# Optimization experiments

Hardware: AMD Instinct MI355X
Metric: run time of the kernel (lower is better)

## Reference

```python
import jax, jax.numpy as jnp
import numpy as np

N = 100000
E = 1600000
IN_C, HID_C, OUT_C = 128, 128, 64


def setup_inputs() -> dict:
    key = jax.random.key(0)
    k1, k2, k3, k4 = jax.random.split(key, 4)
    x = jax.random.normal(k1, (N, IN_C), dtype=jnp.float32)
    edge_index = jax.random.randint(k2, (2, E), 0, N, dtype=jnp.int32)
    # Glorot-ish scaled weights
    W1 = jax.random.normal(k3, (IN_C, HID_C), dtype=jnp.float32) / np.sqrt(IN_C)
    b1 = jnp.zeros((HID_C,), dtype=jnp.float32)
    W2 = jax.random.normal(k4, (HID_C, OUT_C), dtype=jnp.float32) / np.sqrt(HID_C)
    b2 = jnp.zeros((OUT_C,), dtype=jnp.float32)
    return {"x": x, "edge_index": edge_index, "W1": W1, "b1": b1, "W2": W2, "b2": b2}


def _gcn_norm(edge_index, num_nodes):
    """Add self loops and compute symmetric D^{-1/2} A D^{-1/2} edge weights (PyG GCNConv defaults)."""
    loop = jnp.arange(num_nodes, dtype=edge_index.dtype)
    row = jnp.concatenate([edge_index[0], loop])  # source nodes
    col = jnp.concatenate([edge_index[1], loop])  # target nodes
    ones = jnp.ones_like(col, dtype=jnp.float32)
    deg = jax.ops.segment_sum(ones, col, num_segments=num_nodes)
    deg_inv_sqrt = jnp.where(deg > 0, jax.lax.rsqrt(jnp.maximum(deg, 1.0)), 0.0)
    norm = deg_inv_sqrt[row] * deg_inv_sqrt[col]  # [E+N]
    return row, col, norm


def _gcn_layer(x, row, col, norm, W, b, num_nodes):
    h = x @ W                                   # [N, C_out] transform first (PyG order)
    msg = h[row] * norm[:, None]                # gather + scale  [E+N, C_out]
    out = jax.ops.segment_sum(msg, col, num_segments=num_nodes)  # scatter-add
    return out + b


def reference(x, edge_index, W1, b1, W2, b2):
    row, col, norm = _gcn_norm(edge_index, N)
    h = jax.nn.relu(_gcn_layer(x, row, col, norm, W1, b1, N))
    return _gcn_layer(h, row, col, norm, W2, b2, N)
```

## Files before the change

kernel.cpp:

```cpp
#include <hip/hip_runtime.h>
#include <hip/hip_fp16.h>

#define NODES 100000
#define EDGES 1600000

#define BSHIFT 9
#define BNODES 512
#define NBUCK ((NODES + BNODES - 1) / BNODES)
#define BCAP 10240

#define GB 782
#define SC 1563

typedef __attribute__((ext_vector_type(8))) short short8;
typedef __attribute__((ext_vector_type(8))) _Float16 half8;
typedef __attribute__((ext_vector_type(4))) float f32x4;

__device__ inline unsigned short f2bf(float f) {
    unsigned u = __builtin_bit_cast(unsigned, f);
    u = u + 0x7fff + ((u >> 16) & 1);
    return (unsigned short)(u >> 16);
}
__device__ inline float bf2f(unsigned short h) {
    unsigned u = ((unsigned)h) << 16;
    return __builtin_bit_cast(float, u);
}
__device__ inline unsigned short f2h_bits(float f) {
    __half h = __float2half_rn(f);
    return __builtin_bit_cast(unsigned short, h);
}
__device__ inline float h2f(unsigned short bits) {
    return __half2float(__builtin_bit_cast(__half, bits));
}
__device__ inline float2 h2f2(unsigned int bits) {
    __half2 h = __builtin_bit_cast(__half2, bits);
    return __half22float2(h);
}


__global__ __launch_bounds__(256) void prep_kernel(const float* __restrict__ W1,
                                                   const float* __restrict__ W2,
                                                   unsigned short* __restrict__ wh1,
                                                   unsigned short* __restrict__ wl1,
                                                   unsigned short* __restrict__ w2f,
                                                   int* __restrict__ gcur) {
    const int tid = threadIdx.x;
    const int b = blockIdx.x;
    if (b < 8) {
        constexpr int NCT = 8;
        int idx = b * 256 + tid;
        int lane = idx & 63;
        int rem = idx >> 6;
        int ct = rem % NCT;
        int kt = rem / NCT;
        int kbase = kt * 32 + ((lane >> 4) * 8);
        int c = ct * 16 + (lane & 15);
#pragma unroll
        for (int i = 0; i < 8; i++) {
            float v = W1[(size_t)(kbase + i) * 128 + c];
            unsigned short hi = f2bf(v);
            unsigned short lo = f2bf(v - bf2f(hi));
            wh1[(size_t)idx * 8 + i] = hi;
            wl1[(size_t)idx * 8 + i] = lo;
        }
    } else if (b < 12) {
        constexpr int NCT = 4;
        int idx = (b - 8) * 256 + tid;
        int lane = idx & 63;
        int rem = idx >> 6;
        int ct = rem % NCT;
        int kt = rem / NCT;
        int kbase = kt * 32 + ((lane >> 4) * 8);
        int c = ct * 16 + (lane & 15);
#pragma unroll
        for (int i = 0; i < 8; i++) {
            w2f[(size_t)idx * 8 + i] = f2h_bits(W2[(size_t)(kbase + i) * 64 + c]);
        }
    } else {
        if (tid < NBUCK) gcur[tid] = 0;
    }
}


__device__ __forceinline__ void gemm1_body(const float* __restrict__ X,
                                           const unsigned short* __restrict__ wh,
                                           const unsigned short* __restrict__ wl,
                                           unsigned short* __restrict__ H,
                                           unsigned short* s_wh,
                                           unsigned short* s_wl,
                                           int tid, int bid) {
    constexpr int NCT = 8;
    constexpr int FRAGS = 2048;

    const int wave = tid >> 6;
    const int lane = tid & 63;

    const int row0 = bid * 128 + wave * 16 + (lane & 15);
    const bool active = (bid * 128 + wave * 16) < NODES;

    float xs[4][8];
    if (active) {
        const float* xrow = X + (size_t)row0 * 128 + ((lane >> 4) * 8);
#pragma unroll
        for (int kt = 0; kt < 4; kt++) {
            float4 a = *(const float4*)(xrow + kt * 32);
            float4 b = *(const float4*)(xrow + kt * 32 + 4);
            xs[kt][0] = a.x; xs[kt][1] = a.y; xs[kt][2] = a.z; xs[kt][3] = a.w;
            xs[kt][4] = b.x; xs[kt][5] = b.y; xs[kt][6] = b.z; xs[kt][7] = b.w;
        }
    }

#pragma unroll
    for (int j = 0; j < 4; j++) {
        __builtin_amdgcn_global_load_lds((const unsigned int*)((const char*)wh + ((size_t)tid + j * 512) * 16),
                                         (unsigned int*)(s_wh + ((size_t)tid + j * 512) * 8), 16, 0, 0);
        __builtin_amdgcn_global_load_lds((const unsigned int*)((const char*)wl + ((size_t)tid + j * 512) * 16),
                                         (unsigned int*)(s_wl + ((size_t)tid + j * 512) * 8), 16, 0, 0);
    }
    __syncthreads();

    if (!active) return;

    short8 ah[4], al[4];
#pragma unroll
    for (int kt = 0; kt < 4; kt++) {
#pragma unroll
        for (int i = 0; i < 8; i++) {
            unsigned short hi = f2bf(xs[kt][i]);
            unsigned short lo = f2bf(xs[kt][i] - bf2f(hi));
            ah[kt][i] = (short)hi;
            al[kt][i] = (short)lo;
        }
    }

    f32x4 acc[NCT];
#pragma unroll
    for (int ct = 0; ct < NCT; ct++) acc[ct] = (f32x4){0.f, 0.f, 0.f, 0.f};

#pragma unroll
    for (int kt = 0; kt < 4; kt++) {
#pragma unroll
        for (int ct = 0; ct < NCT; ct++) {
            const int fo = ((kt * NCT + ct) * 64 + lane) * 8;
            short8 bh = *(const short8*)&s_wh[fo];
            short8 bl = *(const short8*)&s_wl[fo];
            acc[ct] = __builtin_amdgcn_mfma_f32_16x16x32_bf16(ah[kt], bh, acc[ct], 0, 0, 0);
            acc[ct] = __builtin_amdgcn_mfma_f32_16x16x32_bf16(al[kt], bh, acc[ct], 0, 0, 0);
            acc[ct] = __builtin_amdgcn_mfma_f32_16x16x32_bf16(ah[kt], bl, acc[ct], 0, 0, 0);
        }
    }

    const int rbase = bid * 128 + wave * 16 + ((lane >> 4) * 4);
#pragma unroll
    for (int ct = 0; ct < NCT; ct++) {
#pragma unroll
        for (int r = 0; r < 4; r++) {
            H[(size_t)(rbase + r) * 128 + ct * 16 + (lane & 15)] = f2h_bits(acc[ct][r]);
        }
    }
}


__global__ __launch_bounds__(512) void gemm1_scatter(const float* __restrict__ X,
                                                     const unsigned short* __restrict__ wh,
                                                     const unsigned short* __restrict__ wl,
                                                     unsigned short* __restrict__ H,
                                                     const int* __restrict__ erow,
                                                     const int* __restrict__ ecol,
                                                     int* __restrict__ gcur,
                                                     int2* __restrict__ temp) {
    __shared__ __align__(16) char smem[65536];
    const int tid = threadIdx.x;

    if (blockIdx.x < GB) {
        unsigned short* s_wh = (unsigned short*)smem;
        unsigned short* s_wl = s_wh + 2048 * 8;
        gemm1_body(X, wh, wl, H, s_wh, s_wl, tid, blockIdx.x);
    } else {
        int* hist = (int*)smem;
        int* rbase = hist + NBUCK;
        const int ebase = (blockIdx.x - GB) * 1024;
        if (tid < NBUCK) hist[tid] = 0;
        __syncthreads();

        const int e0 = ebase + tid;
        const int e1 = ebase + tid + 512;
        const bool v0 = e0 < EDGES;
        const bool v1 = e1 < EDGES;
        int c0 = 0, s0 = 0, b0 = 0, r0 = 0;
        int c1 = 0, s1 = 0, b1 = 0, r1 = 0;
        if (v0) {
            c0 = ecol[e0]; s0 = erow[e0];
            b0 = c0 >> BSHIFT;
            r0 = atomicAdd(&hist[b0], 1);
        }
        if (v1) {
            c1 = ecol[e1]; s1 = erow[e1];
            b1 = c1 >> BSHIFT;
            r1 = atomicAdd(&hist[b1], 1);
        }
        __syncthreads();
        if (tid < NBUCK) {
            int h = hist[tid];
            rbase[tid] = h ? atomicAdd(&gcur[tid], h) : 0;
        }
        __syncthreads();
        if (v0) {
            int2 v; v.x = s0; v.y = c0 & (BNODES - 1);
            temp[(size_t)b0 * BCAP + rbase[b0] + r0] = v;
        }
        if (v1) {
            int2 v; v.x = s1; v.y = c1 & (BNODES - 1);
            temp[(size_t)b1 * BCAP + rbase[b1] + r1] = v;
        }
    }
}


__global__ __launch_bounds__(1024) void bucket_build(const int2* __restrict__ temp,
                                                     const int* __restrict__ gcur,
                                                     int* __restrict__ row_start,
                                                     float* __restrict__ dis,
                                                     int* __restrict__ esrc) {
    __shared__ int cnt[BNODES];
    __shared__ int offs[BNODES];
    __shared__ int cur[BNODES];
    __shared__ int ssc[256];
    const int b = blockIdx.x;
    const int tid = threadIdx.x;

    if (tid < 256) ssc[tid] = (tid < NBUCK) ? gcur[tid] : 0;
    __syncthreads();
    for (int d = 1; d < 256; d <<= 1) {
        int x = (tid < 256 && tid >= d) ? ssc[tid - d] : 0;
        __syncthreads();
        if (tid < 256) ssc[tid] += x;
        __syncthreads();
    }
    const int size = gcur[b];
    const int gbase = ssc[b] - size;
    if (b == 0 && tid == 0) row_start[NODES] = EDGES;

    if (tid < BNODES) cnt[tid] = 0;
    __syncthreads();

    for (int i = tid; i < size; i += 1024) {
        int2 v = temp[(size_t)b * BCAP + i];
        atomicAdd(&cnt[v.y], 1);
    }
    __syncthreads();

    if (tid < BNODES) offs[tid] = cnt[tid];
    __syncthreads();
    for (int d = 1; d < BNODES; d <<= 1) {
        int x = 0;
        if (tid < BNODES && tid >= d) x = offs[tid - d];
        __syncthreads();
        if (tid < BNODES) offs[tid] += x;
        __syncthreads();
    }
    if (tid < BNODES) {
        int excl = offs[tid] - cnt[tid];
        cur[tid] = excl;
        int v = b * BNODES + tid;
        if (v < NODES) {
            row_start[v] = gbase + excl;
            dis[v] = rsqrtf((float)(cnt[tid] + 1));
        }
    }
    __syncthreads();

    for (int i = tid; i < size; i += 1024) {
        int2 v = temp[(size_t)b * BCAP + i];
        int pos = gbase + atomicAdd(&cur[v.y], 1);
        esrc[pos] = v.x;
    }
}


__global__ __launch_bounds__(256, 6) void agg1_gemm2(const unsigned short* __restrict__ H,
                                                     const int* __restrict__ row_start,
                                                     const int* __restrict__ edge_src,
                                                     const float* __restrict__ dis,
                                                     const float* __restrict__ b1,
                                                     const unsigned short* __restrict__ w2f,
                                                     unsigned short* __restrict__ H2) {
    __shared__ float h_lds[16][132];
    __shared__ unsigned short s_w2[1024 * 8];

    const int tid = threadIdx.x;
    const int lane = tid & 63;
    const int sub = lane & 15;
    const int grp = lane >> 4;
    const int nl = (tid >> 6) * 4 + grp;
    const int v = blockIdx.x * 16 + nl;

#pragma unroll
    for (int j = 0; j < 4; j++) {
        __builtin_amdgcn_global_load_lds((const unsigned int*)((const char*)w2f + ((size_t)tid + j * 256) * 16),
                                         (unsigned int*)(s_w2 + ((size_t)tid + j * 256) * 8), 16, 0, 0);
    }

    const uint4* __restrict__ Hq = (const uint4*)H;
    const int e0 = row_start[v];
    const int e1 = row_start[v + 1];
    const float dv = dis[v];

    const float4 ba = ((const float4*)b1)[sub * 2];
    const float4 bb = ((const float4*)b1)[sub * 2 + 1];

    uint4 gs = Hq[(size_t)v * 16 + sub];

    int i0 = edge_src[min(e0 + 0, EDGES - 1)];
    int i1 = edge_src[min(e0 + 1, EDGES - 1)];
    int i2 = edge_src[min(e0 + 2, EDGES - 1)];
    int i3 = edge_src[min(e0 + 3, EDGES - 1)];
    float d0 = dis[i0], d1 = dis[i1], d2 = dis[i2], d3 = dis[i3];

    float a0, a1, a2, a3, a4, a5, a6, a7;
    {
        float2 f0 = h2f2(gs.x), f1 = h2f2(gs.y), f2 = h2f2(gs.z), f3 = h2f2(gs.w);
        a0 = f0.x * dv; a1 = f0.y * dv; a2 = f1.x * dv; a3 = f1.y * dv;
        a4 = f2.x * dv; a5 = f2.y * dv; a6 = f3.x * dv; a7 = f3.y * dv;
    }

    for (int k = e0; k < e1; k += 4) {
        uint4 g0 = Hq[(size_t)i0 * 16 + sub];
        uint4 g1 = Hq[(size_t)i1 * 16 + sub];
        uint4 g2 = Hq[(size_t)i2 * 16 + sub];
        uint4 g3 = Hq[(size_t)i3 * 16 + sub];
        const int n0 = edge_src[min(k + 4, EDGES - 1)];
        const int n1 = edge_src[min(k + 5, EDGES - 1)];
        const int n2 = edge_src[min(k + 6, EDGES - 1)];
        const int n3 = edge_src[min(k + 7, EDGES - 1)];
        const float dn0 = dis[n0], dn1 = dis[n1], dn2 = dis[n2], dn3 = dis[n3];
        const float w0 = d0;
        const float w1 = (k + 1 < e1) ? d1 : 0.f;
        const float w2 = (k + 2 < e1) ? d2 : 0.f;
        const float w3 = (k + 3 < e1) ? d3 : 0.f;
#define ACC(G, W)                                                        \
        {                                                                \
            float2 f0 = h2f2(G.x), f1 = h2f2(G.y);                       \
            float2 f2 = h2f2(G.z), f3 = h2f2(G.w);                       \
            a0 = fmaf(f0.x, W, a0); a1 = fmaf(f0.y, W, a1);              \
            a2 = fmaf(f1.x, W, a2); a3 = fmaf(f1.y, W, a3);              \
            a4 = fmaf(f2.x, W, a4); a5 = fmaf(f2.y, W, a5);              \
            a6 = fmaf(f3.x, W, a6); a7 = fmaf(f3.y, W, a7);              \
        }
        ACC(g0, w0)
        ACC(g1, w1)
        ACC(g2, w2)
        ACC(g3, w3)
#undef ACC
        i0 = n0; i1 = n1; i2 = n2; i3 = n3;
        d0 = dn0; d1 = dn1; d2 = dn2; d3 = dn3;
    }

    {
        float4 oa, ob;
        oa.x = fmaxf(fmaf(a0, dv, ba.x), 0.f);
        oa.y = fmaxf(fmaf(a1, dv, ba.y), 0.f);
        oa.z = fmaxf(fmaf(a2, dv, ba.z), 0.f);
        oa.w = fmaxf(fmaf(a3, dv, ba.w), 0.f);
        ob.x = fmaxf(fmaf(a4, dv, bb.x), 0.f);
        ob.y = fmaxf(fmaf(a5, dv, bb.y), 0.f);
        ob.z = fmaxf(fmaf(a6, dv, bb.z), 0.f);
        ob.w = fmaxf(fmaf(a7, dv, bb.w), 0.f);
        *(float4*)&h_lds[nl][sub * 8] = oa;
        *(float4*)&h_lds[nl][sub * 8 + 4] = ob;
    }
    __syncthreads();

    const int ct = tid >> 6;
    f32x4 acc = (f32x4){0.f, 0.f, 0.f, 0.f};
#pragma unroll
    for (int kt = 0; kt < 4; kt++) {
        const int arow = lane & 15;
        const int acol = (lane >> 4) * 8 + kt * 32;
        float4 pa = *(const float4*)&h_lds[arow][acol];
        float4 pb = *(const float4*)&h_lds[arow][acol + 4];
        half8 af;
        af[0] = (_Float16)pa.x; af[1] = (_Float16)pa.y;
        af[2] = (_Float16)pa.z; af[3] = (_Float16)pa.w;
        af[4] = (_Float16)pb.x; af[5] = (_Float16)pb.y;
        af[6] = (_Float16)pb.z; af[7] = (_Float16)pb.w;
        half8 bf = *(const half8*)&s_w2[((kt * 4 + ct) * 64 + lane) * 8];
        acc = __builtin_amdgcn_mfma_f32_16x16x32_f16(af, bf, acc, 0, 0, 0);
    }

    const int rbase = blockIdx.x * 16 + ((lane >> 4) * 4);
#pragma unroll
    for (int r = 0; r < 4; r++) {
        H2[(size_t)(rbase + r) * 64 + ct * 16 + (lane & 15)] = f2h_bits(acc[r]);
    }
}


__global__ __launch_bounds__(256, 8) void agg_l2(const unsigned short* __restrict__ H,
                                                 const int* __restrict__ row_start,
                                                 const int* __restrict__ edge_src,
                                                 const float* __restrict__ dis,
                                                 const float* __restrict__ bias,
                                                 float* __restrict__ OUT) {
    constexpr int RQ = 8;

    const int lane = threadIdx.x & 63;
    const int sub = lane & 7;
    const int grp = lane >> 3;
    const int wid = (blockIdx.x * 256 + threadIdx.x) >> 6;
    const int v = wid * 8 + grp;

    const uint4* __restrict__ Hq = (const uint4*)H;

    const int e0 = row_start[v];
    const int e1 = row_start[v + 1];
    const float dv = dis[v];

    const float4 ba = ((const float4*)bias)[sub * 2];
    const float4 bb = ((const float4*)bias)[sub * 2 + 1];

    uint4 gs = Hq[(size_t)v * RQ + sub];

    int i0 = edge_src[min(e0 + 0, EDGES - 1)];
    int i1 = edge_src[min(e0 + 1, EDGES - 1)];
    int i2 = edge_src[min(e0 + 2, EDGES - 1)];
    int i3 = edge_src[min(e0 + 3, EDGES - 1)];
    float d0 = dis[i0], d1 = dis[i1], d2 = dis[i2], d3 = dis[i3];

    float a0, a1, a2, a3, a4, a5, a6, a7;
    {
        float2 f0 = h2f2(gs.x), f1 = h2f2(gs.y), f2 = h2f2(gs.z), f3 = h2f2(gs.w);
        a0 = f0.x * dv; a1 = f0.y * dv; a2 = f1.x * dv; a3 = f1.y * dv;
        a4 = f2.x * dv; a5 = f2.y * dv; a6 = f3.x * dv; a7 = f3.y * dv;
    }

    for (int k = e0; k < e1; k += 4) {
        uint4 g0 = Hq[(size_t)i0 * RQ + sub];
        uint4 g1 = Hq[(size_t)i1 * RQ + sub];
        uint4 g2 = Hq[(size_t)i2 * RQ + sub];
        uint4 g3 = Hq[(size_t)i3 * RQ + sub];
        const int n0 = edge_src[min(k + 4, EDGES - 1)];
        const int n1 = edge_src[min(k + 5, EDGES - 1)];
        const int n2 = edge_src[min(k + 6, EDGES - 1)];
        const int n3 = edge_src[min(k + 7, EDGES - 1)];
        const float dn0 = dis[n0], dn1 = dis[n1], dn2 = dis[n2], dn3 = dis[n3];
        const float w0 = d0;
        const float w1 = (k + 1 < e1) ? d1 : 0.f;
        const float w2 = (k + 2 < e1) ? d2 : 0.f;
        const float w3 = (k + 3 < e1) ? d3 : 0.f;
#define ACC(G, W)                                                        \
        {                                                                \
            float2 f0 = h2f2(G.x), f1 = h2f2(G.y);                       \
            float2 f2 = h2f2(G.z), f3 = h2f2(G.w);                       \
            a0 = fmaf(f0.x, W, a0); a1 = fmaf(f0.y, W, a1);              \
            a2 = fmaf(f1.x, W, a2); a3 = fmaf(f1.y, W, a3);              \
            a4 = fmaf(f2.x, W, a4); a5 = fmaf(f2.y, W, a5);              \
            a6 = fmaf(f3.x, W, a6); a7 = fmaf(f3.y, W, a7);              \
        }
        ACC(g0, w0)
        ACC(g1, w1)
        ACC(g2, w2)
        ACC(g3, w3)
#undef ACC
        i0 = n0; i1 = n1; i2 = n2; i3 = n3;
        d0 = dn0; d1 = dn1; d2 = dn2; d3 = dn3;
    }

    float4 oa, ob;
    oa.x = fmaf(a0, dv, ba.x); oa.y = fmaf(a1, dv, ba.y);
    oa.z = fmaf(a2, dv, ba.z); oa.w = fmaf(a3, dv, ba.w);
    ob.x = fmaf(a4, dv, bb.x); ob.y = fmaf(a5, dv, bb.y);
    ob.z = fmaf(a6, dv, bb.z); ob.w = fmaf(a7, dv, bb.w);
    float* outp = OUT + (size_t)v * 64 + sub * 8;
    *(float4*)(outp) = oa;
    *(float4*)(outp + 4) = ob;
}


extern "C" void kernel_launch(void* const* d_in, const int* in_sizes, int n_in,
                              void* d_out, int out_size, void* d_ws, size_t ws_size,
                              hipStream_t stream) {
    const float* x   = (const float*)d_in[0];
    const int* eidx  = (const int*)d_in[1];
    const float* W1  = (const float*)d_in[2];
    const float* b1  = (const float*)d_in[3];
    const float* W2  = (const float*)d_in[4];
    const float* b2  = (const float*)d_in[5];
    float* out = (float*)d_out;

    const int* erow = eidx;
    const int* ecol = eidx + EDGES;

    char* w = (char*)d_ws;
    size_t off = 0;
    auto alloc = [&](size_t bytes) -> void* {
        void* p = w + off;
        off += (bytes + 255) & ~(size_t)255;
        return p;
    };
    float* dis     = (float*)alloc((size_t)NODES * 4);
    int*   rowst   = (int*)alloc((size_t)(NODES + 1) * 4);
    int*   esrc    = (int*)alloc((size_t)EDGES * 4);
    int*   gcur    = (int*)alloc(NBUCK * 4);
    int2*  temp    = (int2*)alloc((size_t)NBUCK * BCAP * 8);
    unsigned short* wh1 = (unsigned short*)alloc(2048 * 8 * 2);
    unsigned short* wl1 = (unsigned short*)alloc(2048 * 8 * 2);
    unsigned short* w2f = (unsigned short*)alloc(1024 * 8 * 2);
    unsigned short* bufA = (unsigned short*)alloc((size_t)NODES * 128 * 2);
    unsigned short* bufC = (unsigned short*)alloc((size_t)NODES * 64 * 2);

    prep_kernel<<<13, 256, 0, stream>>>(W1, W2, wh1, wl1, w2f, gcur);

    gemm1_scatter<<<GB + SC, 512, 0, stream>>>(x, wh1, wl1, bufA, erow, ecol, gcur, temp);

    bucket_build<<<NBUCK, 1024, 0, stream>>>(temp, gcur, rowst, dis, esrc);

    agg1_gemm2<<<NODES / 16, 256, 0, stream>>>(bufA, rowst, esrc, dis, b1, w2f, bufC);

    agg_l2<<<NODES / 32, 256, 0, stream>>>(bufC, rowst, esrc, dis, b2, out);
}
```

Before: 168.1 us.

## Regroup kernels: fuse weight prep with edge scatter, GEMM1 with bucket build

```diff
diff --git a/kernel.cpp b/kernel.cpp
--- a/kernel.cpp
+++ b/kernel.cpp
@@ -9,8 +9,10 @@
 #define NBUCK ((NODES + BNODES - 1) / BNODES)
 #define BCAP 10240
 
+#define PREP_BLKS 6
+#define SC 1563
+#define BUILD_BLKS NBUCK
 #define GB 782
-#define SC 1563
 
 typedef __attribute__((ext_vector_type(8))) short short8;
 typedef __attribute__((ext_vector_type(8))) _Float16 half8;
@@ -38,17 +40,21 @@
 }
 
 
-__global__ __launch_bounds__(256) void prep_kernel(const float* __restrict__ W1,
-                                                   const float* __restrict__ W2,
-                                                   unsigned short* __restrict__ wh1,
-                                                   unsigned short* __restrict__ wl1,
-                                                   unsigned short* __restrict__ w2f,
-                                                   int* __restrict__ gcur) {
+__global__ __launch_bounds__(512) void prep_scatter(const float* __restrict__ W1,
+                                                    const float* __restrict__ W2,
+                                                    unsigned short* __restrict__ wh1,
+                                                    unsigned short* __restrict__ wl1,
+                                                    unsigned short* __restrict__ w2f,
+                                                    const int* __restrict__ erow,
+                                                    const int* __restrict__ ecol,
+                                                    int* __restrict__ gcur,
+                                                    int2* __restrict__ temp) {
     const int tid = threadIdx.x;
     const int b = blockIdx.x;
-    if (b < 8) {
+
+    if (b < 4) {
         constexpr int NCT = 8;
-        int idx = b * 256 + tid;
+        int idx = b * 512 + tid;
         int lane = idx & 63;
         int rem = idx >> 6;
         int ct = rem % NCT;
@@ -63,9 +69,9 @@
             wh1[(size_t)idx * 8 + i] = hi;
             wl1[(size_t)idx * 8 + i] = lo;
         }
-    } else if (b < 12) {
+    } else if (b < PREP_BLKS) {
         constexpr int NCT = 4;
-        int idx = (b - 8) * 256 + tid;
+        int idx = (b - 4) * 512 + tid;
         int lane = idx & 63;
         int rem = idx >> 6;
         int ct = rem % NCT;
@@ -77,109 +83,9 @@
             w2f[(size_t)idx * 8 + i] = f2h_bits(W2[(size_t)(kbase + i) * 64 + c]);
         }
     } else {
-        if (tid < NBUCK) gcur[tid] = 0;
-    }
-}
-
-
-__device__ __forceinline__ void gemm1_body(const float* __restrict__ X,
-                                           const unsigned short* __restrict__ wh,
-                                           const unsigned short* __restrict__ wl,
-                                           unsigned short* __restrict__ H,
-                                           unsigned short* s_wh,
-                                           unsigned short* s_wl,
-                                           int tid, int bid) {
-    constexpr int NCT = 8;
-    constexpr int FRAGS = 2048;
-
-    const int wave = tid >> 6;
-    const int lane = tid & 63;
-
-    const int row0 = bid * 128 + wave * 16 + (lane & 15);
-    const bool active = (bid * 128 + wave * 16) < NODES;
-
-    float xs[4][8];
-    if (active) {
-        const float* xrow = X + (size_t)row0 * 128 + ((lane >> 4) * 8);
-#pragma unroll
-        for (int kt = 0; kt < 4; kt++) {
-            float4 a = *(const float4*)(xrow + kt * 32);
-            float4 b = *(const float4*)(xrow + kt * 32 + 4);
-            xs[kt][0] = a.x; xs[kt][1] = a.y; xs[kt][2] = a.z; xs[kt][3] = a.w;
-            xs[kt][4] = b.x; xs[kt][5] = b.y; xs[kt][6] = b.z; xs[kt][7] = b.w;
-        }
-    }
-
-#pragma unroll
-    for (int j = 0; j < 4; j++) {
-        __builtin_amdgcn_global_load_lds((const unsigned int*)((const char*)wh + ((size_t)tid + j * 512) * 16),
-                                         (unsigned int*)(s_wh + ((size_t)tid + j * 512) * 8), 16, 0, 0);
-        __builtin_amdgcn_global_load_lds((const unsigned int*)((const char*)wl + ((size_t)tid + j * 512) * 16),
-                                         (unsigned int*)(s_wl + ((size_t)tid + j * 512) * 8), 16, 0, 0);
-    }
-    __syncthreads();
-
-    if (!active) return;
-
-    short8 ah[4], al[4];
-#pragma unroll
-    for (int kt = 0; kt < 4; kt++) {
-#pragma unroll
-        for (int i = 0; i < 8; i++) {
-            unsigned short hi = f2bf(xs[kt][i]);
-            unsigned short lo = f2bf(xs[kt][i] - bf2f(hi));
-            ah[kt][i] = (short)hi;
-            al[kt][i] = (short)lo;
-        }
-    }
-
-    f32x4 acc[NCT];
-#pragma unroll
-    for (int ct = 0; ct < NCT; ct++) acc[ct] = (f32x4){0.f, 0.f, 0.f, 0.f};
-
-#pragma unroll
-    for (int kt = 0; kt < 4; kt++) {
-#pragma unroll
-        for (int ct = 0; ct < NCT; ct++) {
-            const int fo = ((kt * NCT + ct) * 64 + lane) * 8;
-            short8 bh = *(const short8*)&s_wh[fo];
-            short8 bl = *(const short8*)&s_wl[fo];
-            acc[ct] = __builtin_amdgcn_mfma_f32_16x16x32_bf16(ah[kt], bh, acc[ct], 0, 0, 0);
-            acc[ct] = __builtin_amdgcn_mfma_f32_16x16x32_bf16(al[kt], bh, acc[ct], 0, 0, 0);
-            acc[ct] = __builtin_amdgcn_mfma_f32_16x16x32_bf16(ah[kt], bl, acc[ct], 0, 0, 0);
-        }
-    }
-
-    const int rbase = bid * 128 + wave * 16 + ((lane >> 4) * 4);
-#pragma unroll
-    for (int ct = 0; ct < NCT; ct++) {
-#pragma unroll
-        for (int r = 0; r < 4; r++) {
-            H[(size_t)(rbase + r) * 128 + ct * 16 + (lane & 15)] = f2h_bits(acc[ct][r]);
-        }
-    }
-}
-
-
-__global__ __launch_bounds__(512) void gemm1_scatter(const float* __restrict__ X,
-                                                     const unsigned short* __restrict__ wh,
-                                                     const unsigned short* __restrict__ wl,
-                                                     unsigned short* __restrict__ H,
-                                                     const int* __restrict__ erow,
-                                                     const int* __restrict__ ecol,
-                                                     int* __restrict__ gcur,
-                                                     int2* __restrict__ temp) {
-    __shared__ __align__(16) char smem[65536];
-    const int tid = threadIdx.x;
-
-    if (blockIdx.x < GB) {
-        unsigned short* s_wh = (unsigned short*)smem;
-        unsigned short* s_wl = s_wh + 2048 * 8;
-        gemm1_body(X, wh, wl, H, s_wh, s_wl, tid, blockIdx.x);
-    } else {
-        int* hist = (int*)smem;
-        int* rbase = hist + NBUCK;
-        const int ebase = (blockIdx.x - GB) * 1024;
+        __shared__ int hist[NBUCK];
+        __shared__ int rbase[NBUCK];
+        const int ebase = (b - PREP_BLKS) * 1024;
         if (tid < NBUCK) hist[tid] = 0;
         __syncthreads();
 
@@ -217,17 +123,108 @@
 }
 
 
-__global__ __launch_bounds__(1024) void bucket_build(const int2* __restrict__ temp,
-                                                     const int* __restrict__ gcur,
-                                                     int* __restrict__ row_start,
-                                                     float* __restrict__ dis,
-                                                     int* __restrict__ esrc) {
-    __shared__ int cnt[BNODES];
-    __shared__ int offs[BNODES];
-    __shared__ int cur[BNODES];
-    __shared__ int ssc[256];
+__device__ __forceinline__ void gemm1_body(const float* __restrict__ X,
+                                           const unsigned short* __restrict__ wh,
+                                           const unsigned short* __restrict__ wl,
+                                           unsigned short* __restrict__ H,
+                                           unsigned short* s_wh,
+                                           unsigned short* s_wl,
+                                           int tid, int bid) {
+    constexpr int NCT = 8;
+
+    const int wave = tid >> 6;
+    const int lane = tid & 63;
+
+    const int row0 = bid * 128 + wave * 16 + (lane & 15);
+    const bool active = (bid * 128 + wave * 16) < NODES;
+
+    float xs[4][8];
+    if (active) {
+        const float* xrow = X + (size_t)row0 * 128 + ((lane >> 4) * 8);
+#pragma unroll
+        for (int kt = 0; kt < 4; kt++) {
+            float4 a = *(const float4*)(xrow + kt * 32);
+            float4 b = *(const float4*)(xrow + kt * 32 + 4);
+            xs[kt][0] = a.x; xs[kt][1] = a.y; xs[kt][2] = a.z; xs[kt][3] = a.w;
+            xs[kt][4] = b.x; xs[kt][5] = b.y; xs[kt][6] = b.z; xs[kt][7] = b.w;
+        }
+    }
+
+#pragma unroll
+    for (int j = 0; j < 4; j++) {
+        __builtin_amdgcn_global_load_lds((const unsigned int*)((const char*)wh + ((size_t)tid + j * 512) * 16),
+                                         (unsigned int*)(s_wh + ((size_t)tid + j * 512) * 8), 16, 0, 0);
+        __builtin_amdgcn_global_load_lds((const unsigned int*)((const char*)wl + ((size_t)tid + j * 512) * 16),
+                                         (unsigned int*)(s_wl + ((size_t)tid + j * 512) * 8), 16, 0, 0);
+    }
+    __syncthreads();
+
+    if (!active) return;
+
+    short8 ah[4], al[4];
+#pragma unroll
+    for (int kt = 0; kt < 4; kt++) {
+#pragma unroll
+        for (int i = 0; i < 8; i++) {
+            unsigned short hi = f2bf(xs[kt][i]);
+            unsigned short lo = f2bf(xs[kt][i] - bf2f(hi));
+            ah[kt][i] = (short)hi;
+            al[kt][i] = (short)lo;
+        }
+    }
+
+    f32x4 acc[NCT];
+#pragma unroll
+    for (int ct = 0; ct < NCT; ct++) acc[ct] = (f32x4){0.f, 0.f, 0.f, 0.f};
+
+#pragma unroll
+    for (int kt = 0; kt < 4; kt++) {
+#pragma unroll
+        for (int ct = 0; ct < NCT; ct++) {
+            const int fo = ((kt * NCT + ct) * 64 + lane) * 8;
+            short8 bh = *(const short8*)&s_wh[fo];
+            short8 bl = *(const short8*)&s_wl[fo];
+            acc[ct] = __builtin_amdgcn_mfma_f32_16x16x32_bf16(ah[kt], bh, acc[ct], 0, 0, 0);
+            acc[ct] = __builtin_amdgcn_mfma_f32_16x16x32_bf16(al[kt], bh, acc[ct], 0, 0, 0);
+            acc[ct] = __builtin_amdgcn_mfma_f32_16x16x32_bf16(ah[kt], bl, acc[ct], 0, 0, 0);
+        }
+    }
+
+    const int rbase = bid * 128 + wave * 16 + ((lane >> 4) * 4);
+#pragma unroll
+    for (int ct = 0; ct < NCT; ct++) {
+#pragma unroll
+        for (int r = 0; r < 4; r++) {
+            H[(size_t)(rbase + r) * 128 + ct * 16 + (lane & 15)] = f2h_bits(acc[ct][r]);
+        }
+    }
+}
+
+
+__global__ __launch_bounds__(512) void gemm1_build(const float* __restrict__ X,
+                                                   const unsigned short* __restrict__ wh,
+                                                   const unsigned short* __restrict__ wl,
+                                                   unsigned short* __restrict__ H,
+                                                   const int2* __restrict__ temp,
+                                                   const int* __restrict__ gcur,
+                                                   int* __restrict__ row_start,
+                                                   float* __restrict__ dis,
+                                                   int* __restrict__ esrc) {
+    __shared__ __align__(16) char smem[65536];
+    const int tid = threadIdx.x;
+
+    if (blockIdx.x >= BUILD_BLKS) {
+        unsigned short* s_wh = (unsigned short*)smem;
+        unsigned short* s_wl = s_wh + 2048 * 8;
+        gemm1_body(X, wh, wl, H, s_wh, s_wl, tid, blockIdx.x - BUILD_BLKS);
+        return;
+    }
+
+    int* cnt = (int*)smem;
+    int* offs = cnt + BNODES;
+    int* cur = offs + BNODES;
+    int* ssc = cur + BNODES;
     const int b = blockIdx.x;
-    const int tid = threadIdx.x;
 
     if (tid < 256) ssc[tid] = (tid < NBUCK) ? gcur[tid] : 0;
     __syncthreads();
@@ -241,25 +238,24 @@
     const int gbase = ssc[b] - size;
     if (b == 0 && tid == 0) row_start[NODES] = EDGES;
 
-    if (tid < BNODES) cnt[tid] = 0;
-    __syncthreads();
-
-    for (int i = tid; i < size; i += 1024) {
+    cnt[tid] = 0;
+    __syncthreads();
+
+    for (int i = tid; i < size; i += 512) {
         int2 v = temp[(size_t)b * BCAP + i];
         atomicAdd(&cnt[v.y], 1);
     }
     __syncthreads();
 
-    if (tid < BNODES) offs[tid] = cnt[tid];
+    offs[tid] = cnt[tid];
     __syncthreads();
     for (int d = 1; d < BNODES; d <<= 1) {
-        int x = 0;
-        if (tid < BNODES && tid >= d) x = offs[tid - d];
-        __syncthreads();
-        if (tid < BNODES) offs[tid] += x;
-        __syncthreads();
-    }
-    if (tid < BNODES) {
+        int x = (tid >= d) ? offs[tid - d] : 0;
+        __syncthreads();
+        offs[tid] += x;
+        __syncthreads();
+    }
+    {
         int excl = offs[tid] - cnt[tid];
         cur[tid] = excl;
         int v = b * BNODES + tid;
@@ -270,7 +266,7 @@
     }
     __syncthreads();
 
-    for (int i = tid; i < size; i += 1024) {
+    for (int i = tid; i < size; i += 512) {
         int2 v = temp[(size_t)b * BCAP + i];
         int pos = gbase + atomicAdd(&cur[v.y], 1);
         esrc[pos] = v.x;
@@ -509,11 +505,13 @@
     unsigned short* bufA = (unsigned short*)alloc((size_t)NODES * 128 * 2);
     unsigned short* bufC = (unsigned short*)alloc((size_t)NODES * 64 * 2);
 
-    prep_kernel<<<13, 256, 0, stream>>>(W1, W2, wh1, wl1, w2f, gcur);
-
-    gemm1_scatter<<<GB + SC, 512, 0, stream>>>(x, wh1, wl1, bufA, erow, ecol, gcur, temp);
-
-    bucket_build<<<NBUCK, 1024, 0, stream>>>(temp, gcur, rowst, dis, esrc);
+    hipMemsetAsync(gcur, 0, NBUCK * 4, stream);
+
+    prep_scatter<<<PREP_BLKS + SC, 512, 0, stream>>>(W1, W2, wh1, wl1, w2f,
+                                                     erow, ecol, gcur, temp);
+
+    gemm1_build<<<BUILD_BLKS + GB, 512, 0, stream>>>(x, wh1, wl1, bufA,
+                                                     temp, gcur, rowst, dis, esrc);
 
     agg1_gemm2<<<NODES / 16, 256, 0, stream>>>(bufA, rowst, esrc, dis, b1, w2f, bufC);
 
```

Result: slower. 174.8 us (+4.0%).
